# Kernel optimization log

Measured on AMD Instinct MI355X. Metric: run time of the kernel, lower is better.

## Reference

```python
import math
import jax, jax.numpy as jnp
import numpy as np

B, T, C = 4, 2048, 1024
N_HEAD = 16
HEAD_DIM = C // N_HEAD

def setup_inputs() -> dict:
    key = jax.random.key(0)
    k0, k1, k2, k3, k4 = jax.random.split(key, 5)
    s = 1.0 / math.sqrt(C)
    return {
        "x": jax.random.normal(k0, (B, T, C), dtype=jnp.float32),
        "W_q": jax.random.normal(k1, (C, C), dtype=jnp.float32) * s,
        "W_k": jax.random.normal(k2, (C, C), dtype=jnp.float32) * s,
        "W_v": jax.random.normal(k3, (C, C), dtype=jnp.float32) * s,
        "W_o": jax.random.normal(k4, (C, C), dtype=jnp.float32) * s,
    }

def reference(x, W_q, W_k, W_v, W_o):
    b, t, c = x.shape
    h, hd = N_HEAD, HEAD_DIM
    # nn.Linear(y) = y @ W.T ; project and split heads -> [B, H, T, hd]
    q = (x @ W_q.T).reshape(b, t, h, hd).transpose(0, 2, 1, 3)
    k = (x @ W_k.T).reshape(b, t, h, hd).transpose(0, 2, 1, 3)
    v = (x @ W_v.T).reshape(b, t, h, hd).transpose(0, 2, 1, 3)
    # scores [B, H, T, T], causal mask, stable softmax
    attn = jnp.einsum('bhqd,bhkd->bhqk', q, k) / math.sqrt(hd)
    causal = jnp.tril(jnp.ones((t, t), dtype=bool))
    attn = jnp.where(causal[None, None], attn, -jnp.inf)
    attn = jax.nn.softmax(attn, axis=-1)
    out = jnp.einsum('bhqk,bhkd->bhqd', attn, v)
    out = out.transpose(0, 2, 1, 3).reshape(b, t, c)
    return out @ W_o.T
```

## Files before the change

### kernel.cpp

```cpp
#include <hip/hip_runtime.h>
#include <math.h>

#define Bsz 4
#define Tsz 2048
#define Csz 1024
#define NH  16
#define HD  64

typedef short bf16x8 __attribute__((ext_vector_type(8)));
typedef float f32x4  __attribute__((ext_vector_type(4)));
typedef unsigned short u16;
typedef unsigned int uint;

__device__ __forceinline__ u16 f2bf(float f) {
    union { float f; unsigned u; } v; v.f = f;
    unsigned r = v.u + 0x7fffu + ((v.u >> 16) & 1u);
    return (u16)(r >> 16);
}

__device__ __forceinline__ uint pkbf(float a, float b) {
    union { float f; uint u; } x, y; x.f = a; y.f = b;
    return ((x.u + 0x8000u) >> 16) | ((y.u + 0x8000u) & 0xFFFF0000u);
}

__global__ void cast_kernel(const float* __restrict__ src, u16* __restrict__ dst, int n) {
    int i = (blockIdx.x * blockDim.x + threadIdx.x) * 8;
    if (i + 8 <= n) {
        float4 a = *(const float4*)(src + i);
        float4 b = *(const float4*)(src + i + 4);
        bf16x8 o;
        o[0] = (short)f2bf(a.x); o[1] = (short)f2bf(a.y);
        o[2] = (short)f2bf(a.z); o[3] = (short)f2bf(a.w);
        o[4] = (short)f2bf(b.x); o[5] = (short)f2bf(b.y);
        o[6] = (short)f2bf(b.z); o[7] = (short)f2bf(b.w);
        *(bf16x8*)(dst + i) = o;
    } else {
        for (; i < n; i++) dst[i] = f2bf(src[i]);
    }
}

__global__ void cast3_kernel(const float* __restrict__ s0, const float* __restrict__ s1,
                             const float* __restrict__ s2, u16* __restrict__ dst) {
    const int NW = Csz * Csz;
    int i = (blockIdx.x * blockDim.x + threadIdx.x) * 8;
    int m = i >> 20;
    int local = i & (NW - 1);
    const float* src = (m == 0) ? s0 : (m == 1) ? s1 : s2;
    float4 a = *(const float4*)(src + local);
    float4 b = *(const float4*)(src + local + 4);
    bf16x8 o;
    o[0] = (short)f2bf(a.x); o[1] = (short)f2bf(a.y);
    o[2] = (short)f2bf(a.z); o[3] = (short)f2bf(a.w);
    o[4] = (short)f2bf(b.x); o[5] = (short)f2bf(b.y);
    o[6] = (short)f2bf(b.z); o[7] = (short)f2bf(b.w);
    *(bf16x8*)(dst + i) = o;
}

#define GEMM_PIPELINE_BODY(A_, B_, K_)                                               \
    __shared__ u16 sA[128 * 32];                                                     \
    __shared__ u16 sB[128 * 32];                                                     \
    const int tid  = threadIdx.x;                                                    \
    const int wave = tid >> 6, lane = tid & 63;                                      \
    const int lr = lane & 15, lq = lane >> 4;                                        \
    const int m0 = blockIdx.y * 128, n0 = blockIdx.x * 128;                          \
    const int wm = (wave & 1) * 64, wn = (wave >> 1) * 64;                           \
    const int srow = lane >> 2;                                                      \
    const int scol = (lane & 3) * 8;                                                 \
    const u16* gA = (A_) + (size_t)(m0 + wave * 32 + srow) * (K_) + scol;            \
    const u16* gB = (B_) + (size_t)(n0 + wave * 32 + srow) * (K_) + scol;            \
    u16* lA0 = sA + wave * 1024 + srow * 32 + scol;                                  \
    u16* lA1 = lA0 + 16 * 32;                                                        \
    u16* lB0 = sB + wave * 1024 + srow * 32 + scol;                                  \
    u16* lB1 = lB0 + 16 * 32;                                                        \
    f32x4 acc[4][4] = {};                                                            \
    bf16x8 pA0 = *(const bf16x8*)(gA);                                               \
    bf16x8 pA1 = *(const bf16x8*)(gA + (size_t)16 * (K_));                           \
    bf16x8 pB0 = *(const bf16x8*)(gB);                                               \
    bf16x8 pB1 = *(const bf16x8*)(gB + (size_t)16 * (K_));                           \
    for (int k0 = 0; k0 < (K_); k0 += 32) {                                          \
        __syncthreads();                                                             \
        *(bf16x8*)lA0 = pA0; *(bf16x8*)lA1 = pA1;                                    \
        *(bf16x8*)lB0 = pB0; *(bf16x8*)lB1 = pB1;                                    \
        __syncthreads();                                                             \
        if (k0 + 32 < (K_)) {                                                        \
            pA0 = *(const bf16x8*)(gA + k0 + 32);                                    \
            pA1 = *(const bf16x8*)(gA + (size_t)16 * (K_) + k0 + 32);                \
            pB0 = *(const bf16x8*)(gB + k0 + 32);                                    \
            pB1 = *(const bf16x8*)(gB + (size_t)16 * (K_) + k0 + 32);                \
        }                                                                            \
        bf16x8 af[4], bfv[4];                                                        \
        _Pragma("unroll")                                                            \
        for (int f = 0; f < 4; f++)                                                  \
            af[f]  = *(const bf16x8*)(sA + (wm + f * 16 + lr) * 32 + lq * 8);        \
        _Pragma("unroll")                                                            \
        for (int f = 0; f < 4; f++)                                                  \
            bfv[f] = *(const bf16x8*)(sB + (wn + f * 16 + lr) * 32 + lq * 8);        \
        _Pragma("unroll")                                                            \
        for (int i = 0; i < 4; i++)                                                  \
            _Pragma("unroll")                                                        \
            for (int j = 0; j < 4; j++)                                              \
                acc[i][j] = __builtin_amdgcn_mfma_f32_16x16x32_bf16(af[i], bfv[j], acc[i][j], 0, 0, 0); \
    }

__global__ __launch_bounds__(256, 2)
void gemm_qkv(const u16* __restrict__ A, const u16* __restrict__ Bm,
              u16* __restrict__ Qo, u16* __restrict__ Ko, u16* __restrict__ Vo,
              float qscale) {
    GEMM_PIPELINE_BODY(A, Bm, Csz)

    const int sel = n0 >> 10;
    if (sel == 2) {
        #pragma unroll
        for (int i = 0; i < 4; i++) {
            #pragma unroll
            for (int j = 0; j < 4; j++) {
                int m = m0 + wm + i * 16 + lq * 4;
                int b = m >> 11, t = m & (Tsz - 1);
                int n = (n0 & 1023) + wn + j * 16 + lr;
                int h = n >> 6, d = n & (HD - 1);
                uint2 pk;
                pk.x = pkbf(acc[i][j][0], acc[i][j][1]);
                pk.y = pkbf(acc[i][j][2], acc[i][j][3]);
                *(uint2*)(&Vo[(((size_t)b * NH + h) * HD + d) * Tsz + t]) = pk;
            }
        }
    } else {
        const float scale = (sel == 0) ? qscale : 1.0f;
        u16* dst = (sel == 0) ? Qo : Ko;
        #pragma unroll
        for (int i = 0; i < 4; i++)
            #pragma unroll
            for (int j = 0; j < 4; j++)
                #pragma unroll
                for (int r = 0; r < 4; r++) {
                    int m = m0 + wm + i * 16 + lq * 4 + r;
                    int n = (n0 & 1023) + wn + j * 16 + lr;
                    int b = m >> 11, t = m & (Tsz - 1);
                    int h = n >> 6,  d = n & (HD - 1);
                    dst[(((size_t)b * NH + h) * Tsz + t) * HD + d] = f2bf(acc[i][j][r] * scale);
                }
    }
}

__global__ __launch_bounds__(256, 2)
void gemm_out(const u16* __restrict__ A, const u16* __restrict__ Bm,
              float* __restrict__ out) {
    GEMM_PIPELINE_BODY(A, Bm, Csz)

    #pragma unroll
    for (int i = 0; i < 4; i++)
        #pragma unroll
        for (int j = 0; j < 4; j++)
            #pragma unroll
            for (int r = 0; r < 4; r++) {
                int m = m0 + wm + i * 16 + lq * 4 + r;
                int n = n0 + wn + j * 16 + lr;
                out[(size_t)m * Csz + n] = acc[i][j][r];
            }
}

#define LDT 72

__global__ __launch_bounds__(256, 4)
void attn_kernel(const u16* __restrict__ Q, const u16* __restrict__ Kb,
                 const u16* __restrict__ Vt, u16* __restrict__ O) {
    __shared__ u16 sK[64 * LDT];
    __shared__ u16 sV[64 * LDT];
    __shared__ u16 sP[4][16 * LDT];
    const int tid  = threadIdx.x;
    const int wave = tid >> 6, lane = tid & 63;
    const int lr = lane & 15, lq = lane >> 4;
    const int bh = blockIdx.y;
    const int qa = blockIdx.x;
    const int qc = 31 - qa;
    const int ta = qa * 64, tc = qc * 64;

    const u16* Qp = Q  + (size_t)bh * Tsz * HD;
    const u16* Kp = Kb + (size_t)bh * Tsz * HD;
    const u16* Vp = Vt + (size_t)bh * HD * Tsz;

    bf16x8 qfA0 = *(const bf16x8*)(Qp + (size_t)(ta + wave * 16 + lr) * HD + lq * 8);
    bf16x8 qfA1 = *(const bf16x8*)(Qp + (size_t)(ta + wave * 16 + lr) * HD + 32 + lq * 8);
    bf16x8 qfC0 = *(const bf16x8*)(Qp + (size_t)(tc + wave * 16 + lr) * HD + lq * 8);
    bf16x8 qfC1 = *(const bf16x8*)(Qp + (size_t)(tc + wave * 16 + lr) * HD + 32 + lq * 8);

    f32x4 accOA[4] = {}, accOC[4] = {};
    f32x4 accLA = {}, accLC = {};

    bf16x8 ones;
    #pragma unroll
    for (int i = 0; i < 8; i++) ones[i] = (short)0x3F80;

#define PROCESS(T0, QF0, QF1, ACCO, ACCL, DIAG)                                       \
    {                                                                                 \
        f32x4 accS[4];                                                                \
        _Pragma("unroll")                                                             \
        for (int j = 0; j < 4; j++) {                                                 \
            bf16x8 b0 = *(const bf16x8*)(sK + (j * 16 + lr) * LDT + lq * 8);          \
            bf16x8 b1 = *(const bf16x8*)(sK + (j * 16 + lr) * LDT + 32 + lq * 8);     \
            f32x4 z = {};                                                             \
            z = __builtin_amdgcn_mfma_f32_16x16x32_bf16(QF0, b0, z, 0, 0, 0);         \
            z = __builtin_amdgcn_mfma_f32_16x16x32_bf16(QF1, b1, z, 0, 0, 0);         \
            accS[j] = z;                                                              \
        }                                                                             \
        _Pragma("unroll")                                                             \
        for (int r = 0; r < 4; r++) {                                                 \
            const int rowg = (T0) + wave * 16 + lq * 4 + r;                           \
            _Pragma("unroll")                                                         \
            for (int j = 0; j < 4; j++) {                                             \
                float v = accS[j][r];                                                 \
                if (DIAG && (kb * 64 + j * 16 + lr > rowg)) v = -200.0f;              \
                sP[wave][(lq * 4 + r) * LDT + j * 16 + lr] =                          \
                    f2bf(__builtin_amdgcn_exp2f(v));                                  \
            }                                                                         \
        }                                                                             \
        _Pragma("unroll")                                                             \
        for (int ks = 0; ks < 2; ks++) {                                              \
            bf16x8 pf = *(const bf16x8*)(&sP[wave][0] + lr * LDT + ks * 32 + lq * 8); \
            ACCL = __builtin_amdgcn_mfma_f32_16x16x32_bf16(pf, ones, ACCL, 0, 0, 0);  \
            _Pragma("unroll")                                                         \
            for (int j = 0; j < 4; j++) {                                             \
                bf16x8 vf = *(const bf16x8*)(sV + (j * 16 + lr) * LDT + ks * 32 + lq * 8); \
                ACCO[j] = __builtin_amdgcn_mfma_f32_16x16x32_bf16(pf, vf, ACCO[j], 0, 0, 0); \
            }                                                                         \
        }                                                                             \
    }

    for (int kb = 0; kb <= qc; kb++) {
        __syncthreads();
        #pragma unroll
        for (int c = tid; c < 512; c += 256) {
            int row = c >> 3, dc = (c & 7) * 8;
            *(bf16x8*)(sK + row * LDT + dc) =
                *(const bf16x8*)(Kp + (size_t)(kb * 64 + row) * HD + dc);
            *(bf16x8*)(sV + row * LDT + dc) =
                *(const bf16x8*)(Vp + (size_t)row * Tsz + kb * 64 + dc);
        }
        __syncthreads();
        if (kb <= qa) PROCESS(ta, qfA0, qfA1, accOA, accLA, (kb == qa));
        PROCESS(tc, qfC0, qfC1, accOC, accLC, (kb == qc));
    }
#undef PROCESS

    const int b = bh >> 4, h = bh & 15;
    #pragma unroll
    for (int j = 0; j < 4; j++) {
        #pragma unroll
        for (int r = 0; r < 4; r++) {
            int t = wave * 16 + lq * 4 + r;
            int d = j * 16 + lr;
            O[((size_t)b * Tsz + ta + t) * Csz + h * HD + d] = f2bf(accOA[j][r] / accLA[r]);
            O[((size_t)b * Tsz + tc + t) * Csz + h * HD + d] = f2bf(accOC[j][r] / accLC[r]);
        }
    }
}

extern "C" void kernel_launch(void* const* d_in, const int* in_sizes, int n_in,
                              void* d_out, int out_size, void* d_ws, size_t ws_size,
                              hipStream_t stream) {
    const float* x  = (const float*)d_in[0];
    const float* Wq = (const float*)d_in[1];
    const float* Wk = (const float*)d_in[2];
    const float* Wv = (const float*)d_in[3];
    const float* Wo = (const float*)d_in[4];
    float* out = (float*)d_out;

    const size_t NX = (size_t)Bsz * Tsz * Csz;
    const size_t NW = (size_t)Csz * Csz;

    char* ws = (char*)d_ws;
    u16* xb   = (u16*)ws; ws += NX * 2;
    u16* wqkv = (u16*)ws; ws += 3 * NW * 2;
    u16* wob  = (u16*)ws; ws += NW * 2;
    u16* qbuf = (u16*)ws; ws += NX * 2;
    u16* kbuf = (u16*)ws; ws += NX * 2;
    u16* vtb  = (u16*)ws; ws += NX * 2;
    u16* abuf = (u16*)ws; ws += NX * 2;

    cast_kernel<<<dim3((unsigned)(NX / 2048)), 256, 0, stream>>>(x, xb, (int)NX);
    cast3_kernel<<<dim3((unsigned)(3 * NW / 2048)), 256, 0, stream>>>(Wq, Wk, Wv, wqkv);
    cast_kernel<<<dim3((unsigned)(NW / 2048)), 256, 0, stream>>>(Wo, wob, (int)NW);

    const float qscale = 0.125f * 1.44269504088896340736f;
    gemm_qkv<<<dim3(24, 64), 256, 0, stream>>>(xb, wqkv, qbuf, kbuf, vtb, qscale);

    attn_kernel<<<dim3(16, Bsz * NH), 256, 0, stream>>>(qbuf, kbuf, vtb, abuf);

    gemm_out<<<dim3(8, 64), 256, 0, stream>>>(abuf, wob, out);
}
```

Baseline: 276.7 us.

## Double-buffer GEMM LDS, pad attention P tile, truncate exp, merge weight casts

The GEMM main loop now alternates between two LDS buffers, which removes one __syncthreads per k-step. The attention P scratch tile gets a narrower row stride (68 instead of 72). The exp2 result is truncated to bf16 instead of rounded. The four weight casts are merged into one launch. These target barrier overhead, LDS bank conflicts, conversion ALU work and launch count. Costs are double the GEMM LDS, which may lower occupancy, and slightly biased bf16 truncation of the softmax probabilities. The merged cast assumes wob directly follows wqkv in the workspace, which the layout satisfies.

```diff
diff --git a/kernel.cpp b/kernel.cpp
--- a/kernel.cpp
+++ b/kernel.cpp
@@ -39,13 +39,14 @@
     }
 }
 
-__global__ void cast3_kernel(const float* __restrict__ s0, const float* __restrict__ s1,
-                             const float* __restrict__ s2, u16* __restrict__ dst) {
+__global__ void cast4_kernel(const float* __restrict__ s0, const float* __restrict__ s1,
+                             const float* __restrict__ s2, const float* __restrict__ s3,
+                             u16* __restrict__ dst) {
     const int NW = Csz * Csz;
     int i = (blockIdx.x * blockDim.x + threadIdx.x) * 8;
     int m = i >> 20;
     int local = i & (NW - 1);
-    const float* src = (m == 0) ? s0 : (m == 1) ? s1 : s2;
+    const float* src = (m == 0) ? s0 : (m == 1) ? s1 : (m == 2) ? s2 : s3;
     float4 a = *(const float4*)(src + local);
     float4 b = *(const float4*)(src + local + 4);
     bf16x8 o;
@@ -57,8 +58,8 @@
 }
 
 #define GEMM_PIPELINE_BODY(A_, B_, K_)                                               \
-    __shared__ u16 sA[128 * 32];                                                     \
-    __shared__ u16 sB[128 * 32];                                                     \
+    __shared__ u16 sA[2][128 * 32];                                                  \
+    __shared__ u16 sB[2][128 * 32];                                                  \
     const int tid  = threadIdx.x;                                                    \
     const int wave = tid >> 6, lane = tid & 63;                                      \
     const int lr = lane & 15, lq = lane >> 4;                                        \
@@ -68,19 +69,18 @@
     const int scol = (lane & 3) * 8;                                                 \
     const u16* gA = (A_) + (size_t)(m0 + wave * 32 + srow) * (K_) + scol;            \
     const u16* gB = (B_) + (size_t)(n0 + wave * 32 + srow) * (K_) + scol;            \
-    u16* lA0 = sA + wave * 1024 + srow * 32 + scol;                                  \
-    u16* lA1 = lA0 + 16 * 32;                                                        \
-    u16* lB0 = sB + wave * 1024 + srow * 32 + scol;                                  \
-    u16* lB1 = lB0 + 16 * 32;                                                        \
+    const int soff = wave * 1024 + srow * 32 + scol;                                 \
     f32x4 acc[4][4] = {};                                                            \
     bf16x8 pA0 = *(const bf16x8*)(gA);                                               \
     bf16x8 pA1 = *(const bf16x8*)(gA + (size_t)16 * (K_));                           \
     bf16x8 pB0 = *(const bf16x8*)(gB);                                               \
     bf16x8 pB1 = *(const bf16x8*)(gB + (size_t)16 * (K_));                           \
+    int buf = 0;                                                                     \
     for (int k0 = 0; k0 < (K_); k0 += 32) {                                          \
-        __syncthreads();                                                             \
-        *(bf16x8*)lA0 = pA0; *(bf16x8*)lA1 = pA1;                                    \
-        *(bf16x8*)lB0 = pB0; *(bf16x8*)lB1 = pB1;                                    \
+        u16* dA = &sA[buf][0] + soff;                                                \
+        u16* dB = &sB[buf][0] + soff;                                                \
+        *(bf16x8*)dA = pA0; *(bf16x8*)(dA + 512) = pA1;                              \
+        *(bf16x8*)dB = pB0; *(bf16x8*)(dB + 512) = pB1;                              \
         __syncthreads();                                                             \
         if (k0 + 32 < (K_)) {                                                        \
             pA0 = *(const bf16x8*)(gA + k0 + 32);                                    \
@@ -88,18 +88,21 @@
             pB0 = *(const bf16x8*)(gB + k0 + 32);                                    \
             pB1 = *(const bf16x8*)(gB + (size_t)16 * (K_) + k0 + 32);                \
         }                                                                            \
+        const u16* rA = &sA[buf][0];                                                 \
+        const u16* rB = &sB[buf][0];                                                 \
         bf16x8 af[4], bfv[4];                                                        \
         _Pragma("unroll")                                                            \
         for (int f = 0; f < 4; f++)                                                  \
-            af[f]  = *(const bf16x8*)(sA + (wm + f * 16 + lr) * 32 + lq * 8);        \
+            af[f]  = *(const bf16x8*)(rA + (wm + f * 16 + lr) * 32 + lq * 8);        \
         _Pragma("unroll")                                                            \
         for (int f = 0; f < 4; f++)                                                  \
-            bfv[f] = *(const bf16x8*)(sB + (wn + f * 16 + lr) * 32 + lq * 8);        \
+            bfv[f] = *(const bf16x8*)(rB + (wn + f * 16 + lr) * 32 + lq * 8);        \
         _Pragma("unroll")                                                            \
         for (int i = 0; i < 4; i++)                                                  \
             _Pragma("unroll")                                                        \
             for (int j = 0; j < 4; j++)                                              \
                 acc[i][j] = __builtin_amdgcn_mfma_f32_16x16x32_bf16(af[i], bfv[j], acc[i][j], 0, 0, 0); \
+        buf ^= 1;                                                                    \
     }
 
 __global__ __launch_bounds__(256, 2)
@@ -159,14 +162,15 @@
             }
 }
 
-#define LDT 72
+#define LDT  72
+#define LDTP 68
 
 __global__ __launch_bounds__(256, 4)
 void attn_kernel(const u16* __restrict__ Q, const u16* __restrict__ Kb,
                  const u16* __restrict__ Vt, u16* __restrict__ O) {
     __shared__ u16 sK[64 * LDT];
     __shared__ u16 sV[64 * LDT];
-    __shared__ u16 sP[4][16 * LDT];
+    __shared__ u16 sP[4][16 * LDTP];
     const int tid  = threadIdx.x;
     const int wave = tid >> 6, lane = tid & 63;
     const int lr = lane & 15, lq = lane >> 4;
@@ -210,13 +214,14 @@
             for (int j = 0; j < 4; j++) {                                             \
                 float v = accS[j][r];                                                 \
                 if (DIAG && (kb * 64 + j * 16 + lr > rowg)) v = -200.0f;              \
-                sP[wave][(lq * 4 + r) * LDT + j * 16 + lr] =                          \
-                    f2bf(__builtin_amdgcn_exp2f(v));                                  \
+                union { float f; uint u; } e;                                         \
+                e.f = __builtin_amdgcn_exp2f(v);                                      \
+                sP[wave][(lq * 4 + r) * LDTP + j * 16 + lr] = (u16)(e.u >> 16);       \
             }                                                                         \
         }                                                                             \
         _Pragma("unroll")                                                             \
         for (int ks = 0; ks < 2; ks++) {                                              \
-            bf16x8 pf = *(const bf16x8*)(&sP[wave][0] + lr * LDT + ks * 32 + lq * 8); \
+            bf16x8 pf = *(const bf16x8*)(&sP[wave][0] + lr * LDTP + ks * 32 + lq * 8);\
             ACCL = __builtin_amdgcn_mfma_f32_16x16x32_bf16(pf, ones, ACCL, 0, 0, 0);  \
             _Pragma("unroll")                                                         \
             for (int j = 0; j < 4; j++) {                                             \
@@ -278,8 +283,7 @@
     u16* abuf = (u16*)ws; ws += NX * 2;
 
     cast_kernel<<<dim3((unsigned)(NX / 2048)), 256, 0, stream>>>(x, xb, (int)NX);
-    cast3_kernel<<<dim3((unsigned)(3 * NW / 2048)), 256, 0, stream>>>(Wq, Wk, Wv, wqkv);
-    cast_kernel<<<dim3((unsigned)(NW / 2048)), 256, 0, stream>>>(Wo, wob, (int)NW);
+    cast4_kernel<<<dim3((unsigned)(4 * NW / 2048)), 256, 0, stream>>>(Wq, Wk, Wv, Wo, wqkv);
 
     const float qscale = 0.125f * 1.44269504088896340736f;
     gemm_qkv<<<dim3(24, 64), 256, 0, stream>>>(xb, wqkv, qbuf, kbuf, vtb, qscale);
```

Result: no change. 272.5 us (-1.5%).
